# Kernel tuning notes

Measured on AMD Instinct MI355X. Metric: run time of the kernel, lower is better.

Reference implementation:

```python
import math
import jax, jax.numpy as jnp
import numpy as np

N, D, K = 8192, 256, 32


def setup_inputs() -> dict:
    key = jax.random.key(0)
    kx, kw, kb = jax.random.split(key, 3)
    x = jax.random.normal(kx, (N, D), dtype=jnp.float32)
    # params per _init_weights: w ~ N(1, 0.01), b ~ N(0, 0.01)
    w = 1.0 + 0.01 * jax.random.normal(kw, (K, D), dtype=jnp.float32)
    b = 0.01 * jax.random.normal(kb, (K, D), dtype=jnp.float32)
    return {"x": x, "w": w, "b": b}


def reference(x, w, b):
    # x: (N, D); w, b: (K, D)
    y1 = w[None, :, :] * (x[:, None, :] + b[None, :, :])        # (N, K, D)
    y2 = y1 * y1                                                 # (N, K, D)
    y4 = -0.5 * jnp.sum(y2, axis=-1)                             # (N, K)
    gamma = jax.nn.softmax(y4, axis=-1)                          # (N, K)
    y6 = (y2 - 1.0) * (1.0 / math.sqrt(2.0))                     # (N, K, D)
    g = gamma[:, :, None]                                        # (N, K, 1)
    n, kk, d = y1.shape
    sigma_part = (g * y6).reshape(n, kk * d)                     # (N, K*D)
    mu_part = (g * y1).reshape(n, kk * d)                        # (N, K*D)
    phi_patches = jnp.concatenate([sigma_part, mu_part], axis=-1)
    return jnp.mean(phi_patches, axis=0)                         # (2*K*D,)
```

## Files before the change

### kernel.cpp

```cpp
#include <hip/hip_runtime.h>
#include <math.h>

#define Nn 8192
#define Dd 256
#define Kk 32

typedef float        f4x __attribute__((ext_vector_type(4)));
typedef unsigned int u2x __attribute__((ext_vector_type(2)));
typedef unsigned int u4x __attribute__((ext_vector_type(4)));

#define SP_OFF  2228224

__device__ __forceinline__ unsigned bfpack(float a, float b) {
    unsigned ua = __float_as_uint(a); ua += 0x7FFFu + ((ua >> 16) & 1u);
    unsigned ub = __float_as_uint(b); ub += 0x7FFFu + ((ub >> 16) & 1u);
    return (ua >> 16) | (ub & 0xFFFF0000u);
}
__device__ __forceinline__ void nt_store_bf4(unsigned short* p, f4x v) {
    u2x d2; d2.x = bfpack(v.x, v.y); d2.y = bfpack(v.z, v.w);
    __builtin_nontemporal_store(d2, (u2x*)p);
}
__device__ __forceinline__ float bflo(unsigned u) { return __uint_as_float(u << 16); }
__device__ __forceinline__ float bfhi(unsigned u) { return __uint_as_float(u & 0xFFFF0000u); }

__global__ __launch_bounds__(1024) void fused_kernel(const float* __restrict__ x,
                                                     const float* __restrict__ w,
                                                     const float* __restrict__ b,
                                                     float* __restrict__ ws,
                                                     float* __restrict__ out) {
    __shared__ __align__(16) float4 uS4[64 * 33];
    __shared__ __align__(16) float4 vS4[64 * 33];
    __shared__ __align__(16) float4 xS4[32 * 64];
    __shared__ float  gS[1024];

    float* Sp = ws + SP_OFF;
    int tid = threadIdx.x;
    int blk = blockIdx.x;

    if (tid < 64) out[blk * 64 + tid] = 0.f;

    {
        const float* xg = x + (size_t)blk * 32 * Dd;
        #pragma unroll
        for (int i = 0; i < 2; ++i) {
            int e4 = tid + i * 1024;
            __builtin_amdgcn_global_load_lds(
                (const __attribute__((address_space(1))) void*)(xg + (size_t)e4 * 4),
                (__attribute__((address_space(3))) void*)(&xS4[e4]),
                16, 0, 0);
        }
    }

    {
        const float4* w4 = (const float4*)w;
        const float4* b4 = (const float4*)b;
        #pragma unroll
        for (int i = 0; i < 2; ++i) {
            int e4 = tid + i * 1024;
            int k  = e4 >> 6;
            int d4 = e4 & 63;
            float4 wv = w4[e4];
            float4 bv = b4[e4];
            float4 vv = {wv.x * bv.x, wv.y * bv.y, wv.z * bv.z, wv.w * bv.w};
            uS4[d4 * 33 + k] = wv;
            vS4[d4 * 33 + k] = vv;
        }
    }
    __syncthreads();

    {
        int lane = tid & 63;
        int wave = tid >> 6;
        int k = lane & 31;
        int h = lane >> 5;
        int r0 = wave * 2;

        const float4* xr0 = &xS4[(r0 + 0) * 64];
        const float4* xr1 = &xS4[(r0 + 1) * 64];

        float4 a0 = {0.f, 0.f, 0.f, 0.f}, a1 = a0;

        #pragma unroll 8
        for (int i = 0; i < 32; ++i) {
            int ii = h * 32 + i;
            float4 u  = uS4[ii * 33 + k];
            float4 v  = vS4[ii * 33 + k];
            float4 x0 = xr0[ii];
            float4 x1 = xr1[ii];
            float y;
            y = fmaf(u.x, x0.x, v.x); a0.x = fmaf(y, y, a0.x);
            y = fmaf(u.y, x0.y, v.y); a0.y = fmaf(y, y, a0.y);
            y = fmaf(u.z, x0.z, v.z); a0.z = fmaf(y, y, a0.z);
            y = fmaf(u.w, x0.w, v.w); a0.w = fmaf(y, y, a0.w);
            y = fmaf(u.x, x1.x, v.x); a1.x = fmaf(y, y, a1.x);
            y = fmaf(u.y, x1.y, v.y); a1.y = fmaf(y, y, a1.y);
            y = fmaf(u.z, x1.z, v.z); a1.z = fmaf(y, y, a1.z);
            y = fmaf(u.w, x1.w, v.w); a1.w = fmaf(y, y, a1.w);
        }

        float s0 = (a0.x + a0.y) + (a0.z + a0.w);
        float s1 = (a1.x + a1.y) + (a1.z + a1.w);
        s0 += __shfl_xor(s0, 32);
        s1 += __shfl_xor(s1, 32);
        float y40 = -0.5f * s0, y41 = -0.5f * s1;

        float m0 = y40, m1 = y41;
        #pragma unroll
        for (int o = 16; o >= 1; o >>= 1) {
            m0 = fmaxf(m0, __shfl_xor(m0, o));
            m1 = fmaxf(m1, __shfl_xor(m1, o));
        }
        float e0 = __expf(y40 - m0), e1 = __expf(y41 - m1);
        float t0 = e0, t1 = e1;
        #pragma unroll
        for (int o = 16; o >= 1; o >>= 1) {
            t0 += __shfl_xor(t0, o);
            t1 += __shfl_xor(t1, o);
        }
        if (h == 0) {
            gS[(r0 + 0) * 32 + k] = e0 / t0;
            gS[(r0 + 1) * 32 + k] = e1 / t1;
        }
    }
    __syncthreads();

    if (tid < 32) {
        float s0 = 0.f, s1 = 0.f, s2 = 0.f, s3 = 0.f;
        #pragma unroll
        for (int r = 0; r < 32; r += 4) {
            s0 += gS[(r + 0) * 32 + tid];
            s1 += gS[(r + 1) * 32 + tid];
            s2 += gS[(r + 2) * 32 + tid];
            s3 += gS[(r + 3) * 32 + tid];
        }
        Sp[tid * 256 + blk] = (s0 + s1) + (s2 + s3);
    }

    {
        int kg = tid >> 6;
        int d4 = tid & 63;
        const f4x* xl4 = (const f4x*)xS4;
        const float2* gS2 = (const float2*)gS;

        f4x aG0 = {0.f, 0.f, 0.f, 0.f}, aH0 = aG0, aG1 = aG0, aH1 = aG0;

        #pragma unroll 4
        for (int r = 0; r < 32; ++r) {
            f4x xv = xl4[r * 64 + d4];
            f4x xx = xv * xv;
            float2 g2 = gS2[r * 16 + kg];
            aG0 += g2.x * xv;  aH0 += g2.x * xx;
            aG1 += g2.y * xv;  aH1 += g2.y * xx;
        }

        unsigned short* Pb = (unsigned short*)ws;
        int k0 = kg * 2, k1 = k0 + 1;
        size_t dd = (size_t)4 * d4;
        nt_store_bf4(Pb + ((size_t)(k0 * 2 + 0) * 256 + blk) * 256 + dd, aG0);
        nt_store_bf4(Pb + ((size_t)(k0 * 2 + 1) * 256 + blk) * 256 + dd, aH0);
        nt_store_bf4(Pb + ((size_t)(k1 * 2 + 0) * 256 + blk) * 256 + dd, aG1);
        nt_store_bf4(Pb + ((size_t)(k1 * 2 + 1) * 256 + blk) * 256 + dd, aH1);
    }
}

__global__ __launch_bounds__(256) void red_final(const float* __restrict__ w,
                                                 const float* __restrict__ b,
                                                 const float* __restrict__ ws,
                                                 float* __restrict__ out) {
    const unsigned short* Pb = (const unsigned short*)ws;
    const float* Sp = ws + SP_OFF;
    __shared__ __align__(16) f4x sT[512];
    __shared__ float sred[4];
    int tid = threadIdx.x;
    int cb = tid & 31;
    int g  = tid >> 5;
    int bid = blockIdx.x;
    int k  = bid >> 4;
    int gh = (bid >> 3) & 1;
    int c  = bid & 7;

    const u4x* p = (const u4x*)(Pb + ((size_t)bid * 32 + g * 4) * 256 + cb * 8);
    f4x a0 = {0.f, 0.f, 0.f, 0.f}, a1 = a0;
    #pragma unroll
    for (int j = 0; j < 4; ++j) {
        u4x v = __builtin_nontemporal_load(&p[(size_t)j * 32]);
        a0.x += bflo(v.x); a0.y += bfhi(v.x); a0.z += bflo(v.y); a0.w += bfhi(v.y);
        a1.x += bflo(v.z); a1.y += bfhi(v.z); a1.z += bflo(v.w); a1.w += bfhi(v.w);
    }
    sT[(g * 32 + cb) * 2 + 0] = a0;
    sT[(g * 32 + cb) * 2 + 1] = a1;
    __syncthreads();

    int d = tid;
    const float* sTf = (const float*)sT;
    float s = 0.f;
    #pragma unroll
    for (int j = 0; j < 8; ++j) s += sTf[j * 256 + d];

    int idx = k * Dd + d;
    float wv = w[idx], bv = b[idx];
    const float invN = 1.0f / 8192.0f;
    const float c2 = 0.70710678118654752440f * invN;
    float w2 = wv * wv;

    float sg_c, mu_c;
    if (gh == 0) {
        mu_c = wv * s * invN;
        sg_c = w2 * 2.0f * bv * s * c2;
    } else {
        mu_c = 0.f;
        sg_c = w2 * s * c2;
    }

    if (gh == 0 && c == 0) {
        float svp = Sp[k * 256 + tid];
        #pragma unroll
        for (int o = 32; o >= 1; o >>= 1) svp += __shfl_xor(svp, o);
        if ((tid & 63) == 0) sred[tid >> 6] = svp;
        __syncthreads();
        float sv = (sred[0] + sred[1]) + (sred[2] + sred[3]);
        sg_c += (w2 * bv * bv - 1.0f) * sv * c2;
        mu_c += wv * bv * sv * invN;
    }

    atomicAdd(&out[idx], sg_c);
    if (gh == 0) atomicAdd(&out[Kk * Dd + idx], mu_c);
}

extern "C" void kernel_launch(void* const* d_in, const int* in_sizes, int n_in,
                              void* d_out, int out_size, void* d_ws, size_t ws_size,
                              hipStream_t stream) {
    const float* x = (const float*)d_in[0];
    const float* w = (const float*)d_in[1];
    const float* b = (const float*)d_in[2];
    float* out = (float*)d_out;
    float* ws = (float*)d_ws;

    hipLaunchKernelGGL(fused_kernel, dim3(256), dim3(1024), 0, stream, x, w, b, ws, out);
    hipLaunchKernelGGL(red_final,    dim3(512), dim3(256),  0, stream, w, b, ws, out);
}
```

Measured before the change: 76.18 us.

## Reorganize partial-sum workspace layout and simplify reduction kernel indexing

The first kernel now permutes the gamma storage order and assigns each wave a 16-column slice of d across all k. Each wave therefore writes one contiguous 512-element bf16 chunk per block instead of scattered per-k rows. The reduction kernel reads these chunks with 32-bit loads, each thread covering two d values, and drops the shared-memory transpose and barrier. The aim is more coalesced stores and a cheaper reduction, at the cost of a different index mapping that is harder to verify and more atomics per thread.

```diff
diff --git a/kernel.cpp b/kernel.cpp
--- a/kernel.cpp
+++ b/kernel.cpp
@@ -7,7 +7,6 @@
 
 typedef float        f4x __attribute__((ext_vector_type(4)));
 typedef unsigned int u2x __attribute__((ext_vector_type(2)));
-typedef unsigned int u4x __attribute__((ext_vector_type(4)));
 
 #define SP_OFF  2228224
 
@@ -118,48 +117,54 @@
             t1 += __shfl_xor(t1, o);
         }
         if (h == 0) {
-            gS[(r0 + 0) * 32 + k] = e0 / t0;
-            gS[(r0 + 1) * 32 + k] = e1 / t1;
+            int kk = (k & 15) * 2 + (k >> 4);
+            gS[(r0 + 0) * 32 + kk] = e0 / t0;
+            gS[(r0 + 1) * 32 + kk] = e1 / t1;
         }
     }
     __syncthreads();
 
     if (tid < 32) {
+        int kk = (tid & 15) * 2 + (tid >> 4);
         float s0 = 0.f, s1 = 0.f, s2 = 0.f, s3 = 0.f;
         #pragma unroll
         for (int r = 0; r < 32; r += 4) {
-            s0 += gS[(r + 0) * 32 + tid];
-            s1 += gS[(r + 1) * 32 + tid];
-            s2 += gS[(r + 2) * 32 + tid];
-            s3 += gS[(r + 3) * 32 + tid];
+            s0 += gS[(r + 0) * 32 + kk];
+            s1 += gS[(r + 1) * 32 + kk];
+            s2 += gS[(r + 2) * 32 + kk];
+            s3 += gS[(r + 3) * 32 + kk];
         }
         Sp[tid * 256 + blk] = (s0 + s1) + (s2 + s3);
     }
 
     {
-        int kg = tid >> 6;
-        int d4 = tid & 63;
+        int lane = tid & 63;
+        int wave = tid >> 6;
+        int k16 = lane >> 2;
+        int dq  = lane & 3;
         const f4x* xl4 = (const f4x*)xS4;
-        const float2* gS2 = (const float2*)gS;
+        const float2* gP = (const float2*)gS;
 
         f4x aG0 = {0.f, 0.f, 0.f, 0.f}, aH0 = aG0, aG1 = aG0, aH1 = aG0;
 
         #pragma unroll 4
         for (int r = 0; r < 32; ++r) {
-            f4x xv = xl4[r * 64 + d4];
+            f4x xv = xl4[r * 64 + wave * 4 + dq];
             f4x xx = xv * xv;
-            float2 g2 = gS2[r * 16 + kg];
+            float2 g2 = gP[r * 16 + k16];
             aG0 += g2.x * xv;  aH0 += g2.x * xx;
             aG1 += g2.y * xv;  aH1 += g2.y * xx;
         }
 
         unsigned short* Pb = (unsigned short*)ws;
-        int k0 = kg * 2, k1 = k0 + 1;
-        size_t dd = (size_t)4 * d4;
-        nt_store_bf4(Pb + ((size_t)(k0 * 2 + 0) * 256 + blk) * 256 + dd, aG0);
-        nt_store_bf4(Pb + ((size_t)(k0 * 2 + 1) * 256 + blk) * 256 + dd, aH0);
-        nt_store_bf4(Pb + ((size_t)(k1 * 2 + 0) * 256 + blk) * 256 + dd, aG1);
-        nt_store_bf4(Pb + ((size_t)(k1 * 2 + 1) * 256 + blk) * 256 + dd, aH1);
+        size_t base = ((size_t)blk * 16 + wave) * 512;
+        const size_t GHS = (size_t)2097152;
+        int o0 = k16 * 16 + dq * 4;
+        int o1 = (k16 + 16) * 16 + dq * 4;
+        nt_store_bf4(Pb + base + o0,        aG0);
+        nt_store_bf4(Pb + base + o1,        aG1);
+        nt_store_bf4(Pb + base + GHS + o0,  aH0);
+        nt_store_bf4(Pb + base + GHS + o1,  aH1);
     }
 }
 
@@ -167,64 +172,60 @@
                                                  const float* __restrict__ b,
                                                  const float* __restrict__ ws,
                                                  float* __restrict__ out) {
-    const unsigned short* Pb = (const unsigned short*)ws;
+    const unsigned* P32 = (const unsigned*)ws;
     const float* Sp = ws + SP_OFF;
-    __shared__ __align__(16) f4x sT[512];
-    __shared__ float sred[4];
     int tid = threadIdx.x;
-    int cb = tid & 31;
-    int g  = tid >> 5;
     int bid = blockIdx.x;
-    int k  = bid >> 4;
-    int gh = (bid >> 3) & 1;
-    int c  = bid & 7;
-
-    const u4x* p = (const u4x*)(Pb + ((size_t)bid * 32 + g * 4) * 256 + cb * 8);
-    f4x a0 = {0.f, 0.f, 0.f, 0.f}, a1 = a0;
+    int gh  = bid >> 8;
+    int wsl = (bid >> 4) & 15;
+    int c   = bid & 15;
+
+    size_t off = (size_t)gh * 1048576 + (size_t)(c * 16) * 4096 + wsl * 256 + tid;
+    float s0 = 0.f, s1 = 0.f;
     #pragma unroll
-    for (int j = 0; j < 4; ++j) {
-        u4x v = __builtin_nontemporal_load(&p[(size_t)j * 32]);
-        a0.x += bflo(v.x); a0.y += bfhi(v.x); a0.z += bflo(v.y); a0.w += bfhi(v.y);
-        a1.x += bflo(v.z); a1.y += bfhi(v.z); a1.z += bflo(v.w); a1.w += bfhi(v.w);
-    }
-    sT[(g * 32 + cb) * 2 + 0] = a0;
-    sT[(g * 32 + cb) * 2 + 1] = a1;
-    __syncthreads();
-
-    int d = tid;
-    const float* sTf = (const float*)sT;
-    float s = 0.f;
-    #pragma unroll
-    for (int j = 0; j < 8; ++j) s += sTf[j * 256 + d];
-
-    int idx = k * Dd + d;
-    float wv = w[idx], bv = b[idx];
+    for (int j = 0; j < 16; ++j) {
+        unsigned v = __builtin_nontemporal_load(&P32[off + (size_t)j * 4096]);
+        s0 += bflo(v);
+        s1 += bfhi(v);
+    }
+
+    int k  = tid >> 3;
+    int d0 = (tid * 2) & 15;
+    int idx0 = k * Dd + wsl * 16 + d0;
+    float wv0 = w[idx0], wv1 = w[idx0 + 1];
+    float bv0 = b[idx0], bv1 = b[idx0 + 1];
     const float invN = 1.0f / 8192.0f;
     const float c2 = 0.70710678118654752440f * invN;
-    float w2 = wv * wv;
-
-    float sg_c, mu_c;
+    float w20 = wv0 * wv0, w21 = wv1 * wv1;
+
+    float sg0, sg1, mu0 = 0.f, mu1 = 0.f;
     if (gh == 0) {
-        mu_c = wv * s * invN;
-        sg_c = w2 * 2.0f * bv * s * c2;
+        mu0 = wv0 * s0 * invN;         mu1 = wv1 * s1 * invN;
+        sg0 = w20 * 2.0f * bv0 * s0 * c2;  sg1 = w21 * 2.0f * bv1 * s1 * c2;
     } else {
-        mu_c = 0.f;
-        sg_c = w2 * s * c2;
+        sg0 = w20 * s0 * c2;           sg1 = w21 * s1 * c2;
     }
 
     if (gh == 0 && c == 0) {
-        float svp = Sp[k * 256 + tid];
-        #pragma unroll
-        for (int o = 32; o >= 1; o >>= 1) svp += __shfl_xor(svp, o);
-        if ((tid & 63) == 0) sred[tid >> 6] = svp;
-        __syncthreads();
-        float sv = (sred[0] + sred[1]) + (sred[2] + sred[3]);
-        sg_c += (w2 * bv * bv - 1.0f) * sv * c2;
-        mu_c += wv * bv * sv * invN;
-    }
-
-    atomicAdd(&out[idx], sg_c);
-    if (gh == 0) atomicAdd(&out[Kk * Dd + idx], mu_c);
+        int j = tid & 7;
+        float acc = 0.f;
+        #pragma unroll 8
+        for (int i = 0; i < 32; ++i) acc += Sp[k * 256 + j * 32 + i];
+        acc += __shfl_xor(acc, 1);
+        acc += __shfl_xor(acc, 2);
+        acc += __shfl_xor(acc, 4);
+        sg0 += (w20 * bv0 * bv0 - 1.0f) * acc * c2;
+        sg1 += (w21 * bv1 * bv1 - 1.0f) * acc * c2;
+        mu0 += wv0 * bv0 * acc * invN;
+        mu1 += wv1 * bv1 * acc * invN;
+    }
+
+    atomicAdd(&out[idx0],     sg0);
+    atomicAdd(&out[idx0 + 1], sg1);
+    if (gh == 0) {
+        atomicAdd(&out[Kk * Dd + idx0],     mu0);
+        atomicAdd(&out[Kk * Dd + idx0 + 1], mu1);
+    }
 }
 
 extern "C" void kernel_launch(void* const* d_in, const int* in_sizes, int n_in,
```

New measurement: 78.21 us. 1.03x slower.
